# Kernel tuning notes

Measured on AMD Instinct MI355X. Metric: run time of the kernel, lower is better.

The kernel has to match this reference:

```python
import jax, jax.numpy as jnp
import numpy as np

D = 2          # in_out_dim
HID = 64       # hidden_dim of hypernet
WIDTH = 64     # number of rank-1 blocks
COND = 4       # condition_dim
BATCH = 262144
BLOCK = WIDTH * D


def setup_inputs() -> dict:
    key = jax.random.key(0)
    ks = jax.random.split(key, 8)
    s = lambda k, shape, scale: (jax.random.normal(k, shape, jnp.float32) * scale)
    return {
        "t": jax.random.uniform(ks[0], (1,), jnp.float32),
        "z": jax.random.normal(ks[1], (BATCH, D), jnp.float32),
        "logp_z": jnp.zeros((BATCH, 1), jnp.float32),
        "condition": jax.random.normal(ks[2], (BATCH, COND), jnp.float32),
        # HyperNetwork params (torch Linear convention: weight [out, in])
        "hn_w1": s(ks[3], (HID, 1), 1.0), "hn_b1": jnp.zeros((HID,), jnp.float32),
        "hn_w2": s(ks[4], (HID, HID), 1.0 / np.sqrt(HID)), "hn_b2": jnp.zeros((HID,), jnp.float32),
        "hn_w3": s(ks[5], (3 * BLOCK + WIDTH, HID), 1.0 / np.sqrt(HID)), "hn_b3": jnp.zeros((3 * BLOCK + WIDTH,), jnp.float32),
        # TanhSigmoidMultiplyCondition params
        "cl_wz": s(ks[6], (2 * D, D), 1.0 / np.sqrt(D)), "cl_bz": jnp.zeros((2 * D,), jnp.float32),
        "cl_wc": s(ks[7], (2 * D, COND), 1.0 / np.sqrt(COND)), "cl_bc": jnp.zeros((2 * D,), jnp.float32),
    }


def reference(t, z, logp_z, condition, hn_w1, hn_b1, hn_w2, hn_b2, hn_w3, hn_b3,
              cl_wz, cl_bz, cl_wc, cl_bc):
    # --- TanhSigmoidMultiplyCondition: gated fusion of z and condition ---
    in_act = z @ cl_wz.T + cl_bz + condition @ cl_wc.T + cl_bc   # [B, 2D]
    zc = jnp.tanh(in_act[:, :D]) * jax.nn.sigmoid(in_act[:, D:])  # [B, D]

    # --- HyperNetwork: t -> per-block weights W, B, U ---
    p = jnp.tanh(t.reshape(1, 1) @ hn_w1.T + hn_b1)
    p = jnp.tanh(p @ hn_w2.T + hn_b2)
    p = (p @ hn_w3.T + hn_b3).reshape(-1)          # [3*BLOCK + WIDTH]
    W = p[:BLOCK].reshape(WIDTH, D, 1)
    U = p[BLOCK:2 * BLOCK].reshape(WIDTH, 1, D)
    G = p[2 * BLOCK:3 * BLOCK].reshape(WIDTH, 1, D)
    U = U * jax.nn.sigmoid(G)
    Bb = p[3 * BLOCK:].reshape(WIDTH, 1, 1)

    def f(zz):  # velocity field dz/dt as a function of the conditioned z
        h = jnp.tanh(jnp.einsum('bd,wdo->wbo', zz, W) + Bb)  # [WIDTH, B, 1]
        return jnp.einsum('wbo,wod->bd', h, U) / WIDTH        # mean over WIDTH -> [B, D]

    dz_dt = f(zc)

    # trace of Jacobian d(dz_dt)/d(zc) via forward-mode JVPs over the D basis vectors
    eye = jnp.eye(D, dtype=zc.dtype)
    tangents = jax.vmap(
        lambda e: jax.jvp(f, (zc,), (jnp.broadcast_to(e, zc.shape),))[1]
    )(eye)                                   # [D, B, D]
    trace = jnp.einsum('ibi->b', tangents)   # sum of diagonal entries
    dlogp_z_dt = -trace.reshape(-1, 1)       # [B, 1]

    return (dz_dt, dlogp_z_dt, condition)
```

## Files before the change

kernel.cpp:

```cpp
#include <hip/hip_runtime.h>
#include <math.h>

#define D 2
#define HID 64
#define WIDTH 64
#define BATCH 262144
#define BLK 128

typedef float v2f __attribute__((ext_vector_type(2)));

static __device__ __forceinline__ float fexp2(float x){ return __builtin_amdgcn_exp2f(x); }
static __device__ __forceinline__ float frcp(float x){ return __builtin_amdgcn_rcpf(x); }

static __device__ __forceinline__ v2f tanh_pk(v2f x) {
    v2f lo = {-4.f, -4.f}, hi = {4.f, 4.f};
    v2f t = __builtin_elementwise_min(__builtin_elementwise_max(x, lo), hi);
    v2f u = t * t;
    v2f num = t * (945.f + u * (105.f + u));
    v2f den = 945.f + u * (420.f + 15.f * u);
    v2f r; r.x = frcp(den.x); r.y = frcp(den.y);
    return num * r;
}

__global__ __launch_bounds__(256) void fused_ode_kernel(
    const float* __restrict__ t,
    const float* __restrict__ hw1, const float* __restrict__ hb1,
    const float* __restrict__ hw2, const float* __restrict__ hb2,
    const float* __restrict__ hw3, const float* __restrict__ hb3,
    const float* __restrict__ z,
    const float4* __restrict__ c4,
    const float* __restrict__ cl_wz, const float* __restrict__ cl_bz,
    const float* __restrict__ cl_wc, const float* __restrict__ cl_bc,
    float* __restrict__ out)
{
    __shared__ float p1s[HID];
    __shared__ float p2s[HID];
    __shared__ float p3s[3*BLK + WIDTH];
    __shared__ __align__(16) float4 psA[WIDTH];
    __shared__ __align__(8)  float2 psB[WIDTH];
    __shared__ float sSum;

    const int tid = threadIdx.x;
    const int e1 = blockIdx.x * 512 + tid;
    const int e2 = e1 + 256;
    const float L2E = 1.4426950408889634f;

    float2 zA = ((const float2*)z)[e1];
    float2 zB = ((const float2*)z)[e2];
    float4 cA = c4[e1];
    float4 cB = c4[e2];

    if (tid < HID) p1s[tid] = tanhf(t[0]*hw1[tid] + hb1[tid]);
    __syncthreads();

    if (tid < HID) {
        float a0=0.f, a1=0.f, a2=0.f, a3=0.f;
        const float4* row = (const float4*)(hw2 + tid*HID);
        #pragma unroll 4
        for (int k = 0; k < HID/4; ++k) {
            float4 r = row[k];
            a0 = fmaf(p1s[4*k+0], r.x, a0);
            a1 = fmaf(p1s[4*k+1], r.y, a1);
            a2 = fmaf(p1s[4*k+2], r.z, a2);
            a3 = fmaf(p1s[4*k+3], r.w, a3);
        }
        p2s[tid] = tanhf(hb2[tid] + ((a0+a1)+(a2+a3)));
    }
    __syncthreads();

    {
        {
            float a0=0.f, a1=0.f, a2=0.f, a3=0.f;
            const float4* row = (const float4*)(hw3 + tid*HID);
            #pragma unroll 4
            for (int k = 0; k < HID/4; ++k) {
                float4 rv = row[k];
                a0 = fmaf(p2s[4*k+0], rv.x, a0);
                a1 = fmaf(p2s[4*k+1], rv.y, a1);
                a2 = fmaf(p2s[4*k+2], rv.z, a2);
                a3 = fmaf(p2s[4*k+3], rv.w, a3);
            }
            p3s[tid] = hb3[tid] + ((a0+a1)+(a2+a3));
        }
        if (tid < 192) {
            int r2 = 256 + tid;
            float a0=0.f, a1=0.f, a2=0.f, a3=0.f;
            const float4* row = (const float4*)(hw3 + r2*HID);
            #pragma unroll 4
            for (int k = 0; k < HID/4; ++k) {
                float4 rv = row[k];
                a0 = fmaf(p2s[4*k+0], rv.x, a0);
                a1 = fmaf(p2s[4*k+1], rv.y, a1);
                a2 = fmaf(p2s[4*k+2], rv.z, a2);
                a3 = fmaf(p2s[4*k+3], rv.w, a3);
            }
            p3s[r2] = hb3[r2] + ((a0+a1)+(a2+a3));
        }
    }
    __syncthreads();

    if (tid < WIDTH) {
        const int w = tid;
        float W0 = p3s[2*w],        W1 = p3s[2*w+1];
        float U0 = p3s[BLK+2*w],    U1 = p3s[BLK+2*w+1];
        float G0 = p3s[2*BLK+2*w],  G1 = p3s[2*BLK+2*w+1];
        float Bb = p3s[3*BLK+w];
        U0 *= frcp(1.0f + fexp2(-G0*L2E));
        U1 *= frcp(1.0f + fexp2(-G1*L2E));
        float Us0 = U0 * (1.0f/WIDTH);
        float Us1 = U1 * (1.0f/WIDTH);
        float WUs = W0*Us0 + W1*Us1;
        psA[w] = make_float4(W0, W1, Bb, WUs);
        psB[w] = make_float2(Us0, Us1);
        float s = WUs;
        #pragma unroll
        for (int off = 32; off > 0; off >>= 1) s += __shfl_down(s, off);
        if (w == 0) sSum = s;
    }
    __syncthreads();

    float wz[8], wc[16], bbv[4];
    #pragma unroll
    for (int j = 0; j < 8;  ++j) wz[j] = cl_wz[j];
    #pragma unroll
    for (int j = 0; j < 16; ++j) wc[j] = cl_wc[j];
    #pragma unroll
    for (int j = 0; j < 4;  ++j) bbv[j] = cl_bz[j] + cl_bc[j];

    v2f zv0 = {zA.x, zB.x}, zv1 = {zA.y, zB.y};
    v2f cv0 = {cA.x, cB.x}, cv1 = {cA.y, cB.y};
    v2f cv2 = {cA.z, cB.z}, cv3 = {cA.w, cB.w};

    v2f act[4];
    #pragma unroll
    for (int j = 0; j < 4; ++j) {
        v2f a = zv0*wz[2*j] + zv1*wz[2*j+1] + bbv[j];
        a = a + cv0*wc[4*j] + cv1*wc[4*j+1] + cv2*wc[4*j+2] + cv3*wc[4*j+3];
        act[j] = a;
    }
    v2f th0 = tanh_pk(act[0]);
    v2f th1 = tanh_pk(act[1]);
    v2f sg0 = 0.5f + 0.5f*tanh_pk(act[2]*0.5f);
    v2f sg1 = 0.5f + 0.5f*tanh_pk(act[3]*0.5f);
    v2f zc0 = th0 * sg0;
    v2f zc1 = th1 * sg1;

    float4* oc = (float4*)(out + 3*(size_t)BATCH);
    oc[e1] = cA;
    oc[e2] = cB;

    v2f acc0 = {0.f,0.f}, acc1 = {0.f,0.f}, tr = {0.f,0.f};
    #pragma unroll 8
    for (int w = 0; w < WIDTH; ++w) {
        float4 pa = psA[w];
        float2 pb = psB[w];
        v2f pre = zc0*pa.x + zc1*pa.y + pa.z;
        v2f h = tanh_pk(pre);
        acc0 += h * pb.x;
        acc1 += h * pb.y;
        tr   += (h*h) * pa.w;
    }
    float s = sSum;

    ((float2*)out)[e1] = make_float2(acc0.x, acc1.x);
    ((float2*)out)[e2] = make_float2(acc0.y, acc1.y);
    float* dl = out + 2*(size_t)BATCH;
    dl[e1] = tr.x - s;
    dl[e2] = tr.y - s;
}

extern "C" void kernel_launch(void* const* d_in, const int* in_sizes, int n_in,
                              void* d_out, int out_size, void* d_ws, size_t ws_size,
                              hipStream_t stream) {
    const float* t         = (const float*)d_in[0];
    const float* z         = (const float*)d_in[1];
    const float* condition = (const float*)d_in[3];
    const float* hn_w1 = (const float*)d_in[4];
    const float* hn_b1 = (const float*)d_in[5];
    const float* hn_w2 = (const float*)d_in[6];
    const float* hn_b2 = (const float*)d_in[7];
    const float* hn_w3 = (const float*)d_in[8];
    const float* hn_b3 = (const float*)d_in[9];
    const float* cl_wz = (const float*)d_in[10];
    const float* cl_bz = (const float*)d_in[11];
    const float* cl_wc = (const float*)d_in[12];
    const float* cl_bc = (const float*)d_in[13];

    const int block = 256;
    const int grid = BATCH / 512;
    fused_ode_kernel<<<grid, block, 0, stream>>>(
        t, hn_w1, hn_b1, hn_w2, hn_b2, hn_w3, hn_b3,
        z, (const float4*)condition,
        cl_wz, cl_bz, cl_wc, cl_bc, (float*)d_out);
}
```

Before: 21.58 us.

## Split hypernetwork into a single-block kernel and read params from global

Before, every one of the 512 blocks recomputed the three-layer hypernetwork, roughly 28K FMAs plus several barriers per block. Now a single 448-thread block computes it once, writes the per-width parameters and their sum to workspace, and the main ODE kernel reads them from global memory. This adds a second launch and a serial dependency on one tiny kernel. The inner loop also now does uniform global loads (likely scalar or cached) instead of LDS reads.

After: 20.15 us. -6.7%, faster.

```diff
diff --git a/kernel.cpp b/kernel.cpp
--- a/kernel.cpp
+++ b/kernel.cpp
@@ -22,40 +22,25 @@
     return num * r;
 }
 
-__global__ __launch_bounds__(256) void fused_ode_kernel(
+__global__ __launch_bounds__(448) void hyper_kernel(
     const float* __restrict__ t,
-    const float* __restrict__ hw1, const float* __restrict__ hb1,
-    const float* __restrict__ hw2, const float* __restrict__ hb2,
-    const float* __restrict__ hw3, const float* __restrict__ hb3,
-    const float* __restrict__ z,
-    const float4* __restrict__ c4,
-    const float* __restrict__ cl_wz, const float* __restrict__ cl_bz,
-    const float* __restrict__ cl_wc, const float* __restrict__ cl_bc,
-    float* __restrict__ out)
+    const float* __restrict__ w1, const float* __restrict__ b1,
+    const float* __restrict__ w2, const float* __restrict__ b2,
+    const float* __restrict__ w3, const float* __restrict__ b3,
+    float* __restrict__ params)
 {
     __shared__ float p1s[HID];
     __shared__ float p2s[HID];
     __shared__ float p3s[3*BLK + WIDTH];
-    __shared__ __align__(16) float4 psA[WIDTH];
-    __shared__ __align__(8)  float2 psB[WIDTH];
-    __shared__ float sSum;
-
     const int tid = threadIdx.x;
-    const int e1 = blockIdx.x * 512 + tid;
-    const int e2 = e1 + 256;
     const float L2E = 1.4426950408889634f;
 
-    float2 zA = ((const float2*)z)[e1];
-    float2 zB = ((const float2*)z)[e2];
-    float4 cA = c4[e1];
-    float4 cB = c4[e2];
-
-    if (tid < HID) p1s[tid] = tanhf(t[0]*hw1[tid] + hb1[tid]);
+    if (tid < HID) p1s[tid] = tanhf(t[0]*w1[tid] + b1[tid]);
     __syncthreads();
 
     if (tid < HID) {
         float a0=0.f, a1=0.f, a2=0.f, a3=0.f;
-        const float4* row = (const float4*)(hw2 + tid*HID);
+        const float4* row = (const float4*)(w2 + tid*HID);
         #pragma unroll 4
         for (int k = 0; k < HID/4; ++k) {
             float4 r = row[k];
@@ -64,38 +49,22 @@
             a2 = fmaf(p1s[4*k+2], r.z, a2);
             a3 = fmaf(p1s[4*k+3], r.w, a3);
         }
-        p2s[tid] = tanhf(hb2[tid] + ((a0+a1)+(a2+a3)));
+        p2s[tid] = tanhf(b2[tid] + ((a0+a1)+(a2+a3)));
     }
     __syncthreads();
 
     {
-        {
-            float a0=0.f, a1=0.f, a2=0.f, a3=0.f;
-            const float4* row = (const float4*)(hw3 + tid*HID);
-            #pragma unroll 4
-            for (int k = 0; k < HID/4; ++k) {
-                float4 rv = row[k];
-                a0 = fmaf(p2s[4*k+0], rv.x, a0);
-                a1 = fmaf(p2s[4*k+1], rv.y, a1);
-                a2 = fmaf(p2s[4*k+2], rv.z, a2);
-                a3 = fmaf(p2s[4*k+3], rv.w, a3);
-            }
-            p3s[tid] = hb3[tid] + ((a0+a1)+(a2+a3));
+        float a0=0.f, a1=0.f, a2=0.f, a3=0.f;
+        const float4* row = (const float4*)(w3 + tid*HID);
+        #pragma unroll 4
+        for (int k = 0; k < HID/4; ++k) {
+            float4 rv = row[k];
+            a0 = fmaf(p2s[4*k+0], rv.x, a0);
+            a1 = fmaf(p2s[4*k+1], rv.y, a1);
+            a2 = fmaf(p2s[4*k+2], rv.z, a2);
+            a3 = fmaf(p2s[4*k+3], rv.w, a3);
         }
-        if (tid < 192) {
-            int r2 = 256 + tid;
-            float a0=0.f, a1=0.f, a2=0.f, a3=0.f;
-            const float4* row = (const float4*)(hw3 + r2*HID);
-            #pragma unroll 4
-            for (int k = 0; k < HID/4; ++k) {
-                float4 rv = row[k];
-                a0 = fmaf(p2s[4*k+0], rv.x, a0);
-                a1 = fmaf(p2s[4*k+1], rv.y, a1);
-                a2 = fmaf(p2s[4*k+2], rv.z, a2);
-                a3 = fmaf(p2s[4*k+3], rv.w, a3);
-            }
-            p3s[r2] = hb3[r2] + ((a0+a1)+(a2+a3));
-        }
+        p3s[tid] = b3[tid] + ((a0+a1)+(a2+a3));
     }
     __syncthreads();
 
@@ -110,14 +79,31 @@
         float Us0 = U0 * (1.0f/WIDTH);
         float Us1 = U1 * (1.0f/WIDTH);
         float WUs = W0*Us0 + W1*Us1;
-        psA[w] = make_float4(W0, W1, Bb, WUs);
-        psB[w] = make_float2(Us0, Us1);
+        ((float4*)params)[w] = make_float4(W0, W1, Bb, WUs);
+        ((float2*)(params + 256))[w] = make_float2(Us0, Us1);
         float s = WUs;
         #pragma unroll
         for (int off = 32; off > 0; off >>= 1) s += __shfl_down(s, off);
-        if (w == 0) sSum = s;
+        if (w == 0) params[384] = s;
     }
-    __syncthreads();
+}
+
+__global__ __launch_bounds__(256) void ode_kernel(
+    const float* __restrict__ z,
+    const float4* __restrict__ c4,
+    const float* __restrict__ cl_wz, const float* __restrict__ cl_bz,
+    const float* __restrict__ cl_wc, const float* __restrict__ cl_bc,
+    const float* __restrict__ params,
+    float* __restrict__ out)
+{
+    const int tid = threadIdx.x;
+    const int e1 = blockIdx.x * 512 + tid;
+    const int e2 = e1 + 256;
+
+    float2 zA = ((const float2*)z)[e1];
+    float2 zB = ((const float2*)z)[e2];
+    float4 cA = c4[e1];
+    float4 cB = c4[e2];
 
     float wz[8], wc[16], bbv[4];
     #pragma unroll
@@ -149,18 +135,21 @@
     oc[e1] = cA;
     oc[e2] = cB;
 
+    const float4* __restrict__ PA = (const float4*)params;
+    const float2* __restrict__ PB = (const float2*)(params + 256);
+
     v2f acc0 = {0.f,0.f}, acc1 = {0.f,0.f}, tr = {0.f,0.f};
     #pragma unroll 8
     for (int w = 0; w < WIDTH; ++w) {
-        float4 pa = psA[w];
-        float2 pb = psB[w];
+        float4 pa = PA[w];
+        float2 pb = PB[w];
         v2f pre = zc0*pa.x + zc1*pa.y + pa.z;
         v2f h = tanh_pk(pre);
         acc0 += h * pb.x;
         acc1 += h * pb.y;
         tr   += (h*h) * pa.w;
     }
-    float s = sSum;
+    float s = params[384];
 
     ((float2*)out)[e1] = make_float2(acc0.x, acc1.x);
     ((float2*)out)[e2] = make_float2(acc0.y, acc1.y);
@@ -186,10 +175,13 @@
     const float* cl_wc = (const float*)d_in[12];
     const float* cl_bc = (const float*)d_in[13];
 
+    float* params = (float*)d_ws;
+
+    hyper_kernel<<<1, 448, 0, stream>>>(t, hn_w1, hn_b1, hn_w2, hn_b2, hn_w3, hn_b3, params);
+
     const int block = 256;
     const int grid = BATCH / 512;
-    fused_ode_kernel<<<grid, block, 0, stream>>>(
-        t, hn_w1, hn_b1, hn_w2, hn_b2, hn_w3, hn_b3,
+    ode_kernel<<<grid, block, 0, stream>>>(
         z, (const float4*)condition,
-        cl_wz, cl_bz, cl_wc, cl_bc, (float*)d_out);
+        cl_wz, cl_bz, cl_wc, cl_bc, params, (float*)d_out);
 }
```
